# Performance work log

Hardware: AMD Instinct MI355X
Metric: run time of the kernel (lower is better)

## Reference

```python
import jax, jax.numpy as jnp
import numpy as np

NUM_CLASSES = 1000  # label vocabulary size (matches fill_max for label)
B = 16384
D_IN = 1024   # image_embedding
D_OUT = 256   # projection_dim


def setup_inputs() -> dict:
    key = jax.random.key(0)
    k = jax.random.split(key, 6)
    x = jax.random.normal(k[0], (B, D_IN), dtype=jnp.float32)
    label = jax.random.randint(k[1], (B,), 0, NUM_CLASSES, dtype=jnp.int64)
    scale = 1.0 / np.sqrt(D_IN)
    W1_w = jax.random.normal(k[2], (D_OUT, D_IN), dtype=jnp.float32) * scale
    W1_b = jax.random.normal(k[3], (D_OUT,), dtype=jnp.float32) * scale
    W2_w = jax.random.normal(k[4], (D_OUT, D_IN), dtype=jnp.float32) * scale
    W2_b = jax.random.normal(k[5], (D_OUT,), dtype=jnp.float32) * scale
    return {"x": x, "label": label, "W1_w": W1_w, "W1_b": W1_b,
            "W2_w": W2_w, "W2_b": W2_b}


def reference(x, label, W1_w, W1_b, W2_w, W2_b):
    # Leave-one-group-out mean, vectorized via segment sums.
    # Original: for each i, mean of x[label != label_i] (detached); zeros if none.
    b = x.shape[0]
    xd = jax.lax.stop_gradient(x)  # .detach() in the torch code
    label_sum = jax.ops.segment_sum(xd, label, num_segments=NUM_CLASSES)          # [C, D_IN]
    label_cnt = jax.ops.segment_sum(jnp.ones((b,), dtype=x.dtype), label,
                                    num_segments=NUM_CLASSES)                     # [C]
    total_sum = xd.sum(axis=0)                                                    # [D_IN]
    other_sum = total_sum[None, :] - label_sum[label]                             # [B, D_IN]
    other_cnt = jnp.asarray(b, x.dtype) - label_cnt[label]                        # [B]
    calculate_mean = jnp.where(other_cnt[:, None] > 0,
                               other_sum / jnp.maximum(other_cnt, 1)[:, None],
                               jnp.zeros((), x.dtype))                            # [B, D_IN]
    # W1(x) + W2(calculate_mean)  (torch Linear: y = x @ W.T + b)
    return x @ W1_w.T + W1_b + calculate_mean @ W2_w.T + W2_b
```

## Files before the change

### kernel.cpp

```cpp
#include <hip/hip_runtime.h>

constexpr int B      = 16384;
constexpr int D_IN   = 1024;
constexpr int D_OUT  = 256;
constexpr int NCLS   = 1000;

constexpr size_t OFF_WB  = 0;
constexpr size_t OFF_Y1  = OFF_WB + (size_t)512 * D_IN * 2;
constexpr size_t OFF_V   = OFF_Y1 + (size_t)B * D_OUT * 4;
constexpr size_t OFF_U   = OFF_V  + (size_t)1024 * D_OUT * 4;
constexpr size_t OFF_CNT = OFF_U  + 4096;

typedef short bf16x8 __attribute__((ext_vector_type(8)));
typedef float f32x4  __attribute__((ext_vector_type(4)));

__device__ __forceinline__ unsigned short f2bf(float f) {
    unsigned int u = __float_as_uint(f);
    return (unsigned short)((u + 0x7FFFu + ((u >> 16) & 1u)) >> 16);
}

__device__ __forceinline__ void cvt8(const float4& a, const float4& b, unsigned short* dst) {
    union { unsigned short u[8]; bf16x8 v; } r;
    r.u[0] = f2bf(a.x); r.u[1] = f2bf(a.y); r.u[2] = f2bf(a.z); r.u[3] = f2bf(a.w);
    r.u[4] = f2bf(b.x); r.u[5] = f2bf(b.y); r.u[6] = f2bf(b.z); r.u[7] = f2bf(b.w);
    *(bf16x8*)dst = r.v;
}

__device__ __forceinline__ unsigned int cvtpk(float lo, float hi) {
    unsigned int r;
    asm volatile("v_cvt_pk_bf16_f32 %0, %1, %2" : "=v"(r) : "v"(lo), "v"(hi));
    return r;
}

__device__ __forceinline__ void async16(const unsigned short* g, unsigned short* l) {
    __builtin_amdgcn_global_load_lds(
        (const __attribute__((address_space(1))) void*)g,
        (__attribute__((address_space(3))) void*)l,
        16, 0, 0);
}

__global__ __launch_bounds__(256)
void prep_kernel(const float* __restrict__ W1, const float* __restrict__ W2,
                 const int* __restrict__ label,
                 unsigned short* __restrict__ Wb,
                 float* __restrict__ V, float* __restrict__ U, int* __restrict__ cnt) {
    const int blk = blockIdx.x, tid = threadIdx.x;
    if (blk == 0) {
        __shared__ int h[1024];
#pragma unroll
        for (int q = 0; q < 4; ++q) h[q * 256 + tid] = 0;
        __syncthreads();
        for (int base = 0; base < 64; base += 16) {
            int lv[16];
#pragma unroll
            for (int u = 0; u < 16; ++u) lv[u] = label[(base + u) * 256 + tid];
#pragma unroll
            for (int u = 0; u < 16; ++u) atomicAdd(&h[lv[u]], 1);
        }
        __syncthreads();
#pragma unroll
        for (int q = 0; q < 4; ++q) cnt[q * 256 + tid] = h[q * 256 + tid];
    } else if (blk <= 128) {
        int lin = (blk - 1) * 256 + tid;
        int i = lin * 16;
        const float* src = (i < D_OUT * D_IN) ? (W1 + i) : (W2 + (i - D_OUT * D_IN));
        float4 a0 = *(const float4*)(src);
        float4 a1 = *(const float4*)(src + 4);
        float4 a2 = *(const float4*)(src + 8);
        float4 a3 = *(const float4*)(src + 12);
        cvt8(a0, a1, Wb + i);
        cvt8(a2, a3, Wb + i + 8);
    } else {
        int lb = blk - 129;
        int base = (lb * 256 + tid) * 16;
#pragma unroll
        for (int q = 0; q < 4; ++q)
            *(float4*)(V + base + q * 4) = float4{0.f, 0.f, 0.f, 0.f};
        if (lb == 0 && tid < 64)
            *(float4*)(U + tid * 4) = float4{0.f, 0.f, 0.f, 0.f};
    }
}

__global__ __launch_bounds__(256, 2)
void gemm_kernel(const float* __restrict__ x,
                 const unsigned short* __restrict__ Wb,
                 const int* __restrict__ label,
                 float* __restrict__ y1,
                 float* __restrict__ V, float* __restrict__ U) {
    __shared__ unsigned short As[2][128][64];
    __shared__ unsigned short Bs[2][128][64];

    const int tid  = threadIdx.x;
    const int bid  = blockIdx.x;
    const int xcd   = bid & 7;
    const int local = bid >> 3;
    const int bx = xcd * 16 + (local & 15);
    const int by = local >> 4;
    const int bm = bx * 128;
    const int bn = by * 128;

    const int wave = tid >> 6, lane = tid & 63;
    const int quad = lane >> 4, l16 = lane & 15;
    const int wm = (wave >> 1) * 64;
    const int wn = (wave & 1) * 64;
    const int sx = l16 & 7;

    const float* xps[4];
    int adst[4];
#pragma unroll
    for (int rr = 0; rr < 4; ++rr) {
        int dd = rr * 256 + tid;
        int r = dd >> 3, sl = dd & 7;
        int sc = sl ^ (r & 7);
        xps[rr] = x + (size_t)(bm + r) * D_IN + sc * 8;
        adst[rr] = dd * 8;
    }
    const unsigned short* bps[4];
#pragma unroll
    for (int rr = 0; rr < 4; ++rr) {
        int dd = rr * 256 + tid;
        int r = dd >> 3, sl = dd & 7;
        int sc = sl ^ (r & 7);
        bps[rr] = Wb + (size_t)(bn + r) * D_IN + sc * 8;
    }

    f32x4 acc[4][4] = {};
    float4 a0[4], a1[4];

#pragma unroll
    for (int rr = 0; rr < 4; ++rr) {
        a0[rr] = *(const float4*)(xps[rr]);
        a1[rr] = *(const float4*)(xps[rr] + 4);
    }
#pragma unroll
    for (int rr = 0; rr < 4; ++rr)
        async16(bps[rr], &Bs[0][0][0] + rr * 2048 + wave * 512);
#pragma unroll
    for (int rr = 0; rr < 4; ++rr) {
        union { unsigned int w[4]; bf16x8 v; } p;
        p.w[0] = cvtpk(a0[rr].x, a0[rr].y);
        p.w[1] = cvtpk(a0[rr].z, a0[rr].w);
        p.w[2] = cvtpk(a1[rr].x, a1[rr].y);
        p.w[3] = cvtpk(a1[rr].z, a1[rr].w);
        *(bf16x8*)(&As[0][0][0] + adst[rr]) = p.v;
    }

    for (int t = 0; t < 16; ++t) {
        const int cur = t & 1;
        const int k1 = (t + 1) * 64;
        if (t < 15) {
#pragma unroll
            for (int rr = 0; rr < 4; ++rr) {
                a0[rr] = *(const float4*)(xps[rr] + k1);
                a1[rr] = *(const float4*)(xps[rr] + k1 + 4);
            }
            asm volatile("s_waitcnt vmcnt(8)" ::: "memory");
        } else {
            asm volatile("s_waitcnt vmcnt(0)" ::: "memory");
        }
        asm volatile("s_waitcnt lgkmcnt(0)" ::: "memory");
        __builtin_amdgcn_s_barrier();
        __builtin_amdgcn_sched_barrier(0);
        if (t < 15) {
#pragma unroll
            for (int rr = 0; rr < 4; ++rr)
                async16(bps[rr] + k1, &Bs[cur ^ 1][0][0] + rr * 2048 + wave * 512);
        }

#pragma unroll
        for (int ks = 0; ks < 2; ++ks) {
            const int s = ks * 4 + quad;
            bf16x8 af[4], bfr[4];
#pragma unroll
            for (int i = 0; i < 4; ++i)
                af[i] = *(const bf16x8*)&As[cur][wm + i * 16 + l16][((s ^ sx) * 8)];
#pragma unroll
            for (int j = 0; j < 4; ++j)
                bfr[j] = *(const bf16x8*)&Bs[cur][wn + j * 16 + l16][((s ^ sx) * 8)];
#pragma unroll
            for (int i = 0; i < 4; ++i)
#pragma unroll
                for (int j = 0; j < 4; ++j)
                    acc[i][j] = __builtin_amdgcn_mfma_f32_16x16x32_bf16(af[i], bfr[j], acc[i][j], 0, 0, 0);
        }

        if (t < 15) {
#pragma unroll
            for (int rr = 0; rr < 4; ++rr) {
                union { unsigned int w[4]; bf16x8 v; } p;
                p.w[0] = cvtpk(a0[rr].x, a0[rr].y);
                p.w[1] = cvtpk(a0[rr].z, a0[rr].w);
                p.w[2] = cvtpk(a1[rr].x, a1[rr].y);
                p.w[3] = cvtpk(a1[rr].z, a1[rr].w);
                *(bf16x8*)(&As[cur ^ 1][0][0] + adst[rr]) = p.v;
            }
        }
    }

    if (by < 2) {
#pragma unroll
        for (int j = 0; j < 4; ++j) {
            const int n = bn + wn + j * 16 + l16;
#pragma unroll
            for (int i = 0; i < 4; ++i)
#pragma unroll
                for (int r = 0; r < 4; ++r) {
                    const int m = bm + wm + i * 16 + quad * 4 + r;
                    y1[(size_t)m * D_OUT + n] = acc[i][j][r];
                }
        }
    } else {
        int lab[4][4];
#pragma unroll
        for (int i = 0; i < 4; ++i)
#pragma unroll
            for (int r = 0; r < 4; ++r)
                lab[i][r] = label[bm + wm + i * 16 + quad * 4 + r] * D_OUT;

        const int nb = bn - 256;
#pragma unroll
        for (int j = 0; j < 4; ++j) {
            const int n = nb + wn + j * 16 + l16;
            float cs = 0.f;
#pragma unroll
            for (int i = 0; i < 4; ++i)
#pragma unroll
                for (int r = 0; r < 4; ++r) {
                    float v = acc[i][j][r];
                    cs += v;
                    atomicAdd(&V[lab[i][r] + n], v);
                }
            cs += __shfl_xor(cs, 16);
            cs += __shfl_xor(cs, 32);
            if (quad == 0) atomicAdd(&U[n], cs);
        }
    }
}

__global__ __launch_bounds__(256)
void epi_kernel(const float* __restrict__ y1, const float* __restrict__ V,
                const float* __restrict__ U,
                const float* __restrict__ b1, const float* __restrict__ b2,
                const int* __restrict__ cnt, const int* __restrict__ label,
                float* __restrict__ out) {
    const int tid = threadIdx.x;
    const int row = blockIdx.x * 64 + (tid >> 2);
    const int lab = label[row];
    const float inv = 1.0f / (float)(B - cnt[lab]);
    const float* yp = y1 + (size_t)row * D_OUT;
    const float* vp = V  + (size_t)lab * D_OUT;
    float* op = out + (size_t)row * D_OUT;
    const int c0 = (tid & 3) * 4;
#pragma unroll
    for (int it = 0; it < 16; ++it) {
        const int c = c0 + it * 16;
        float4 y = *(const float4*)(yp + c);
        float4 v = *(const float4*)(vp + c);
        float4 u = *(const float4*)(U + c);
        float4 a1 = *(const float4*)(b1 + c);
        float4 a2 = *(const float4*)(b2 + c);
        float4 o;
        o.x = y.x + a1.x + a2.x + (u.x - v.x) * inv;
        o.y = y.y + a1.y + a2.y + (u.y - v.y) * inv;
        o.z = y.z + a1.z + a2.z + (u.z - v.z) * inv;
        o.w = y.w + a1.w + a2.w + (u.w - v.w) * inv;
        *(float4*)(op + c) = o;
    }
}

extern "C" void kernel_launch(void* const* d_in, const int* in_sizes, int n_in,
                              void* d_out, int out_size, void* d_ws, size_t ws_size,
                              hipStream_t stream) {
    const float* x    = (const float*)d_in[0];
    const int*   lab  = (const int*)d_in[1];
    const float* W1_w = (const float*)d_in[2];
    const float* W1_b = (const float*)d_in[3];
    const float* W2_w = (const float*)d_in[4];
    const float* W2_b = (const float*)d_in[5];
    float* out = (float*)d_out;

    char* ws = (char*)d_ws;
    unsigned short* Wb = (unsigned short*)(ws + OFF_WB);
    float* y1 = (float*)(ws + OFF_Y1);
    float* V  = (float*)(ws + OFF_V);
    float* U  = (float*)(ws + OFF_U);
    int*   cnt = (int*)(ws + OFF_CNT);

    prep_kernel<<<193, 256, 0, stream>>>(W1_w, W2_w, lab, Wb, V, U, cnt);
    gemm_kernel<<<512, 256, 0, stream>>>(x, Wb, lab, y1, V, U);
    epi_kernel<<<B / 64, 256, 0, stream>>>(y1, V, U, W1_b, W2_b, cnt, lab, out);
}
```

Measured before the change: 148.8 us.

## Split GEMM into W2 pass emitting bf16 x and fused W1 GEMM epilogue

The single GEMM (W1 and W2 columns together) plus separate epilogue kernel is replaced by two GEMMs. The first computes only the W2 projection, scatters it into per-class and total sums, and writes a bf16 copy of x. The second GEMM reads that bf16 x, computes the W1 projection, and applies the bias and leave-one-group-out mean directly in its epilogue, removing the y1 fp32 intermediate and the epilogue kernel. It adds a 32 MB bf16 x write/read, and the second GEMM uses a simple single-buffered loop with two syncs per k-step and no prefetch overlap.

```diff
diff --git a/kernel.cpp b/kernel.cpp
--- a/kernel.cpp
+++ b/kernel.cpp
@@ -6,10 +6,11 @@
 constexpr int NCLS   = 1000;
 
 constexpr size_t OFF_WB  = 0;
-constexpr size_t OFF_Y1  = OFF_WB + (size_t)512 * D_IN * 2;
-constexpr size_t OFF_V   = OFF_Y1 + (size_t)B * D_OUT * 4;
+constexpr size_t OFF_XB  = OFF_WB + (size_t)512 * D_IN * 2;
+constexpr size_t OFF_V   = OFF_XB + (size_t)B * D_IN * 2;
 constexpr size_t OFF_U   = OFF_V  + (size_t)1024 * D_OUT * 4;
 constexpr size_t OFF_CNT = OFF_U  + 4096;
+constexpr size_t OFF_B12 = OFF_CNT + 4096;
 
 typedef short bf16x8 __attribute__((ext_vector_type(8)));
 typedef float f32x4  __attribute__((ext_vector_type(4)));
@@ -41,9 +42,11 @@
 
 __global__ __launch_bounds__(256)
 void prep_kernel(const float* __restrict__ W1, const float* __restrict__ W2,
+                 const float* __restrict__ b1, const float* __restrict__ b2,
                  const int* __restrict__ label,
                  unsigned short* __restrict__ Wb,
-                 float* __restrict__ V, float* __restrict__ U, int* __restrict__ cnt) {
+                 float* __restrict__ V, float* __restrict__ U,
+                 int* __restrict__ cnt, float* __restrict__ b12) {
     const int blk = blockIdx.x, tid = threadIdx.x;
     if (blk == 0) {
         __shared__ int h[1024];
@@ -60,6 +63,7 @@
         __syncthreads();
 #pragma unroll
         for (int q = 0; q < 4; ++q) cnt[q * 256 + tid] = h[q * 256 + tid];
+        b12[tid] = b1[tid] + b2[tid];
     } else if (blk <= 128) {
         int lin = (blk - 1) * 256 + tid;
         int i = lin * 16;
@@ -82,13 +86,13 @@
 }
 
 __global__ __launch_bounds__(256, 2)
-void gemm_kernel(const float* __restrict__ x,
-                 const unsigned short* __restrict__ Wb,
-                 const int* __restrict__ label,
-                 float* __restrict__ y1,
-                 float* __restrict__ V, float* __restrict__ U) {
+void gemm2_kernel(const float* __restrict__ x,
+                  const unsigned short* __restrict__ Wb,
+                  const int* __restrict__ label,
+                  unsigned short* __restrict__ xb,
+                  float* __restrict__ V, float* __restrict__ U) {
     __shared__ unsigned short As[2][128][64];
-    __shared__ unsigned short Bs[2][128][64];
+    __shared__ unsigned short Bs[2][64][64];
 
     const int tid  = threadIdx.x;
     const int bid  = blockIdx.x;
@@ -97,34 +101,37 @@
     const int bx = xcd * 16 + (local & 15);
     const int by = local >> 4;
     const int bm = bx * 128;
-    const int bn = by * 128;
+    const int bn = by * 64;
 
     const int wave = tid >> 6, lane = tid & 63;
     const int quad = lane >> 4, l16 = lane & 15;
     const int wm = (wave >> 1) * 64;
-    const int wn = (wave & 1) * 64;
+    const int wn = (wave & 1) * 32;
     const int sx = l16 & 7;
 
     const float* xps[4];
+    unsigned short* xbp[4];
     int adst[4];
 #pragma unroll
     for (int rr = 0; rr < 4; ++rr) {
         int dd = rr * 256 + tid;
         int r = dd >> 3, sl = dd & 7;
         int sc = sl ^ (r & 7);
-        xps[rr] = x + (size_t)(bm + r) * D_IN + sc * 8;
+        xps[rr] = x  + (size_t)(bm + r) * D_IN + sc * 8;
+        xbp[rr] = xb + (size_t)(bm + r) * D_IN + sc * 8;
         adst[rr] = dd * 8;
     }
-    const unsigned short* bps[4];
-#pragma unroll
-    for (int rr = 0; rr < 4; ++rr) {
+    const unsigned short* bps[2];
+#pragma unroll
+    for (int rr = 0; rr < 2; ++rr) {
         int dd = rr * 256 + tid;
         int r = dd >> 3, sl = dd & 7;
         int sc = sl ^ (r & 7);
-        bps[rr] = Wb + (size_t)(bn + r) * D_IN + sc * 8;
-    }
-
-    f32x4 acc[4][4] = {};
+        bps[rr] = Wb + (size_t)(256 + bn + r) * D_IN + sc * 8;
+    }
+    const bool emit = (by == 0);
+
+    f32x4 acc[4][2] = {};
     float4 a0[4], a1[4];
 
 #pragma unroll
@@ -133,7 +140,7 @@
         a1[rr] = *(const float4*)(xps[rr] + 4);
     }
 #pragma unroll
-    for (int rr = 0; rr < 4; ++rr)
+    for (int rr = 0; rr < 2; ++rr)
         async16(bps[rr], &Bs[0][0][0] + rr * 2048 + wave * 512);
 #pragma unroll
     for (int rr = 0; rr < 4; ++rr) {
@@ -143,6 +150,7 @@
         p.w[2] = cvtpk(a1[rr].x, a1[rr].y);
         p.w[3] = cvtpk(a1[rr].z, a1[rr].w);
         *(bf16x8*)(&As[0][0][0] + adst[rr]) = p.v;
+        if (emit) *(bf16x8*)(xbp[rr]) = p.v;
     }
 
     for (int t = 0; t < 16; ++t) {
@@ -163,24 +171,24 @@
         __builtin_amdgcn_sched_barrier(0);
         if (t < 15) {
 #pragma unroll
-            for (int rr = 0; rr < 4; ++rr)
+            for (int rr = 0; rr < 2; ++rr)
                 async16(bps[rr] + k1, &Bs[cur ^ 1][0][0] + rr * 2048 + wave * 512);
         }
 
 #pragma unroll
         for (int ks = 0; ks < 2; ++ks) {
             const int s = ks * 4 + quad;
-            bf16x8 af[4], bfr[4];
+            bf16x8 af[4], bfr[2];
 #pragma unroll
             for (int i = 0; i < 4; ++i)
                 af[i] = *(const bf16x8*)&As[cur][wm + i * 16 + l16][((s ^ sx) * 8)];
 #pragma unroll
-            for (int j = 0; j < 4; ++j)
+            for (int j = 0; j < 2; ++j)
                 bfr[j] = *(const bf16x8*)&Bs[cur][wn + j * 16 + l16][((s ^ sx) * 8)];
 #pragma unroll
             for (int i = 0; i < 4; ++i)
 #pragma unroll
-                for (int j = 0; j < 4; ++j)
+                for (int j = 0; j < 2; ++j)
                     acc[i][j] = __builtin_amdgcn_mfma_f32_16x16x32_bf16(af[i], bfr[j], acc[i][j], 0, 0, 0);
         }
 
@@ -193,78 +201,133 @@
                 p.w[2] = cvtpk(a1[rr].x, a1[rr].y);
                 p.w[3] = cvtpk(a1[rr].z, a1[rr].w);
                 *(bf16x8*)(&As[cur ^ 1][0][0] + adst[rr]) = p.v;
+                if (emit) *(bf16x8*)(xbp[rr] + k1) = p.v;
             }
         }
     }
 
-    if (by < 2) {
-#pragma unroll
-        for (int j = 0; j < 4; ++j) {
-            const int n = bn + wn + j * 16 + l16;
+    int lab[4][4];
+#pragma unroll
+    for (int i = 0; i < 4; ++i)
+#pragma unroll
+        for (int r = 0; r < 4; ++r)
+            lab[i][r] = label[bm + wm + i * 16 + quad * 4 + r] * D_OUT;
+
+#pragma unroll
+    for (int j = 0; j < 2; ++j) {
+        const int n = bn + wn + j * 16 + l16;
+        float cs = 0.f;
+#pragma unroll
+        for (int i = 0; i < 4; ++i)
+#pragma unroll
+            for (int r = 0; r < 4; ++r) {
+                float v = acc[i][j][r];
+                cs += v;
+                atomicAdd(&V[lab[i][r] + n], v);
+            }
+        cs += __shfl_xor(cs, 16);
+        cs += __shfl_xor(cs, 32);
+        if (quad == 0) atomicAdd(&U[n], cs);
+    }
+}
+
+__global__ __launch_bounds__(256)
+void gemm1_kernel(const unsigned short* __restrict__ xb,
+                  const unsigned short* __restrict__ Wb,
+                  const int* __restrict__ label,
+                  const float* __restrict__ V, const float* __restrict__ U,
+                  const int* __restrict__ cnt, const float* __restrict__ b12,
+                  float* __restrict__ out) {
+    __shared__ unsigned short As[128][64];
+    __shared__ unsigned short Bs[64][64];
+
+    const int tid  = threadIdx.x;
+    const int bid  = blockIdx.x;
+    const int xcd   = bid & 7;
+    const int local = bid >> 3;
+    const int bx = xcd * 16 + (local & 15);
+    const int by = local >> 4;
+    const int bm = bx * 128;
+    const int bn = by * 64;
+
+    const int wave = tid >> 6, lane = tid & 63;
+    const int quad = lane >> 4, l16 = lane & 15;
+    const int wm = (wave >> 1) * 64;
+    const int wn = (wave & 1) * 32;
+    const int sx = l16 & 7;
+
+    const unsigned short* aps[4];
+#pragma unroll
+    for (int rr = 0; rr < 4; ++rr) {
+        int dd = rr * 256 + tid;
+        int r = dd >> 3, sl = dd & 7;
+        int sc = sl ^ (r & 7);
+        aps[rr] = xb + (size_t)(bm + r) * D_IN + sc * 8;
+    }
+    const unsigned short* bps[2];
+#pragma unroll
+    for (int rr = 0; rr < 2; ++rr) {
+        int dd = rr * 256 + tid;
+        int r = dd >> 3, sl = dd & 7;
+        int sc = sl ^ (r & 7);
+        bps[rr] = Wb + (size_t)(bn + r) * D_IN + sc * 8;
+    }
+
+    f32x4 acc[4][2] = {};
+
+    for (int k0 = 0; k0 < D_IN; k0 += 64) {
+        __syncthreads();
+#pragma unroll
+        for (int rr = 0; rr < 4; ++rr)
+            async16(aps[rr] + k0, &As[0][0] + rr * 2048 + wave * 512);
+#pragma unroll
+        for (int rr = 0; rr < 2; ++rr)
+            async16(bps[rr] + k0, &Bs[0][0] + rr * 2048 + wave * 512);
+        __syncthreads();
+
+#pragma unroll
+        for (int ks = 0; ks < 2; ++ks) {
+            const int s = ks * 4 + quad;
+            bf16x8 af[4], bfr[2];
 #pragma unroll
             for (int i = 0; i < 4; ++i)
-#pragma unroll
-                for (int r = 0; r < 4; ++r) {
-                    const int m = bm + wm + i * 16 + quad * 4 + r;
-                    y1[(size_t)m * D_OUT + n] = acc[i][j][r];
-                }
-        }
-    } else {
-        int lab[4][4];
+                af[i] = *(const bf16x8*)&As[wm + i * 16 + l16][((s ^ sx) * 8)];
+#pragma unroll
+            for (int j = 0; j < 2; ++j)
+                bfr[j] = *(const bf16x8*)&Bs[wn + j * 16 + l16][((s ^ sx) * 8)];
+#pragma unroll
+            for (int i = 0; i < 4; ++i)
+#pragma unroll
+                for (int j = 0; j < 2; ++j)
+                    acc[i][j] = __builtin_amdgcn_mfma_f32_16x16x32_bf16(af[i], bfr[j], acc[i][j], 0, 0, 0);
+        }
+    }
+
+    int lab[4][4];
+    float inv[4][4];
+#pragma unroll
+    for (int i = 0; i < 4; ++i)
+#pragma unroll
+        for (int r = 0; r < 4; ++r) {
+            const int m = bm + wm + i * 16 + quad * 4 + r;
+            const int L = label[m];
+            lab[i][r] = L * D_OUT;
+            inv[i][r] = 1.0f / (float)(B - cnt[L]);
+        }
+
+#pragma unroll
+    for (int j = 0; j < 2; ++j) {
+        const int n = bn + wn + j * 16 + l16;
+        const float un = U[n];
+        const float bb = b12[n];
 #pragma unroll
         for (int i = 0; i < 4; ++i)
 #pragma unroll
-            for (int r = 0; r < 4; ++r)
-                lab[i][r] = label[bm + wm + i * 16 + quad * 4 + r] * D_OUT;
-
-        const int nb = bn - 256;
-#pragma unroll
-        for (int j = 0; j < 4; ++j) {
-            const int n = nb + wn + j * 16 + l16;
-            float cs = 0.f;
-#pragma unroll
-            for (int i = 0; i < 4; ++i)
-#pragma unroll
-                for (int r = 0; r < 4; ++r) {
-                    float v = acc[i][j][r];
-                    cs += v;
-                    atomicAdd(&V[lab[i][r] + n], v);
-                }
-            cs += __shfl_xor(cs, 16);
-            cs += __shfl_xor(cs, 32);
-            if (quad == 0) atomicAdd(&U[n], cs);
-        }
-    }
-}
-
-__global__ __launch_bounds__(256)
-void epi_kernel(const float* __restrict__ y1, const float* __restrict__ V,
-                const float* __restrict__ U,
-                const float* __restrict__ b1, const float* __restrict__ b2,
-                const int* __restrict__ cnt, const int* __restrict__ label,
-                float* __restrict__ out) {
-    const int tid = threadIdx.x;
-    const int row = blockIdx.x * 64 + (tid >> 2);
-    const int lab = label[row];
-    const float inv = 1.0f / (float)(B - cnt[lab]);
-    const float* yp = y1 + (size_t)row * D_OUT;
-    const float* vp = V  + (size_t)lab * D_OUT;
-    float* op = out + (size_t)row * D_OUT;
-    const int c0 = (tid & 3) * 4;
-#pragma unroll
-    for (int it = 0; it < 16; ++it) {
-        const int c = c0 + it * 16;
-        float4 y = *(const float4*)(yp + c);
-        float4 v = *(const float4*)(vp + c);
-        float4 u = *(const float4*)(U + c);
-        float4 a1 = *(const float4*)(b1 + c);
-        float4 a2 = *(const float4*)(b2 + c);
-        float4 o;
-        o.x = y.x + a1.x + a2.x + (u.x - v.x) * inv;
-        o.y = y.y + a1.y + a2.y + (u.y - v.y) * inv;
-        o.z = y.z + a1.z + a2.z + (u.z - v.z) * inv;
-        o.w = y.w + a1.w + a2.w + (u.w - v.w) * inv;
-        *(float4*)(op + c) = o;
+            for (int r = 0; r < 4; ++r) {
+                const int m = bm + wm + i * 16 + quad * 4 + r;
+                out[(size_t)m * D_OUT + n] =
+                    acc[i][j][r] + bb + (un - V[lab[i][r] + n]) * inv[i][r];
+            }
     }
 }
 
@@ -281,12 +344,13 @@
 
     char* ws = (char*)d_ws;
     unsigned short* Wb = (unsigned short*)(ws + OFF_WB);
-    float* y1 = (float*)(ws + OFF_Y1);
-    float* V  = (float*)(ws + OFF_V);
-    float* U  = (float*)(ws + OFF_U);
+    unsigned short* xb = (unsigned short*)(ws + OFF_XB);
+    float* V   = (float*)(ws + OFF_V);
+    float* U   = (float*)(ws + OFF_U);
     int*   cnt = (int*)(ws + OFF_CNT);
-
-    prep_kernel<<<193, 256, 0, stream>>>(W1_w, W2_w, lab, Wb, V, U, cnt);
-    gemm_kernel<<<512, 256, 0, stream>>>(x, Wb, lab, y1, V, U);
-    epi_kernel<<<B / 64, 256, 0, stream>>>(y1, V, U, W1_b, W2_b, cnt, lab, out);
-}
+    float* b12 = (float*)(ws + OFF_B12);
+
+    prep_kernel<<<193, 256, 0, stream>>>(W1_w, W2_w, W1_b, W2_b, lab, Wb, V, U, cnt, b12);
+    gemm2_kernel<<<512, 256, 0, stream>>>(x, Wb, lab, xb, V, U);
+    gemm1_kernel<<<512, 256, 0, stream>>>(xb, Wb, lab, V, U, cnt, b12, out);
+}
```

Result: slower. 155.5 us (+4.5%).
